# Kernel optimization log

Measured on AMD Instinct MI355X. Metric: run time of the kernel, lower is better.

## Reference

```python
import jax, jax.numpy as jnp
import numpy as np

B = 2048
IN_DIM = 98304
H1 = 256
H2 = 32


def setup_inputs() -> dict:
    key = jax.random.key(0)
    ks = jax.random.split(key, 7)
    # x emulates a sparse few-hot HalfKA feature vector: ~32 active features per row
    x = (jax.random.uniform(ks[0], (B, IN_DIM), dtype=jnp.float32) < (32.0 / IN_DIM)).astype(jnp.float32)
    s1 = 1.0 / np.sqrt(IN_DIM)
    s2 = 1.0 / np.sqrt(H1)
    s3 = 1.0 / np.sqrt(H2)
    return {
        "x": x,
        "W1": jax.random.normal(ks[1], (H1, IN_DIM), dtype=jnp.float32) * s1,
        "b1": jax.random.normal(ks[2], (H1,), dtype=jnp.float32) * s1,
        "W2": jax.random.normal(ks[3], (H2, H1), dtype=jnp.float32) * s2,
        "b2": jax.random.normal(ks[4], (H2,), dtype=jnp.float32) * s2,
        "Wout": jax.random.normal(ks[5], (1, H2), dtype=jnp.float32) * s3,
        "bout": jax.random.normal(ks[6], (1,), dtype=jnp.float32) * s3,
    }


def reference(x, W1, b1, W2, b2, Wout, bout):
    # fc1: [B, IN_DIM] @ [IN_DIM, H1] -> [B, H1]  (the sparse-accumulator hotspot)
    h1 = jax.nn.relu(jnp.dot(x, W1.T) + b1)
    h2 = jax.nn.relu(jnp.dot(h1, W2.T) + b2)
    out = jnp.dot(h2, Wout.T) + bout  # [B, 1]
    return out
```

## Files before the change

### kernel.cpp

```cpp
#include <hip/hip_runtime.h>

#define IN_DIM 98304
#define H1 256
#define H2 32
#define NZ_MAX 512
#define TS 64

typedef float f32x4 __attribute__((ext_vector_type(4)));
typedef unsigned short u16;
typedef u16 u16x4 __attribute__((ext_vector_type(4)));

__device__ __forceinline__ u16 f2bf(float f) {
    unsigned u = __builtin_bit_cast(unsigned, f);
    u = (u + 0x7FFFu + ((u >> 16) & 1u)) >> 16;
    return (u16)u;
}
__device__ __forceinline__ float bf2f(u16 h) {
    return __builtin_bit_cast(float, (unsigned)h << 16);
}

__global__ __launch_bounds__(256) void transpose_w1_bf16(const float* __restrict__ W1,
                                                         u16* __restrict__ W1T) {
    __shared__ float tile[TS][TS + 4];
    const int cb = blockIdx.x * TS;
    const int rb = blockIdx.y * TS;
    const int tx = threadIdx.x & 15;
    const int ty = threadIdx.x >> 4;

    #pragma unroll
    for (int rr = 0; rr < 4; ++rr) {
        const int r = rr * 16 + ty;
        f32x4 v = __builtin_nontemporal_load(reinterpret_cast<const f32x4*>(
            &W1[(size_t)(rb + r) * IN_DIM + cb + tx * 4]));
        tile[tx * 4 + 0][r] = v.x;
        tile[tx * 4 + 1][r] = v.y;
        tile[tx * 4 + 2][r] = v.z;
        tile[tx * 4 + 3][r] = v.w;
    }
    __syncthreads();
    #pragma unroll
    for (int cc = 0; cc < 4; ++cc) {
        const int c = cc * 16 + ty;
        u16x4 w;
        w.x = f2bf(tile[c][tx * 4 + 0]);
        w.y = f2bf(tile[c][tx * 4 + 1]);
        w.z = f2bf(tile[c][tx * 4 + 2]);
        w.w = f2bf(tile[c][tx * 4 + 3]);
        *reinterpret_cast<u16x4*>(&W1T[(size_t)(cb + c) * H1 + rb + tx * 4]) = w;
    }
}

template <bool USE_T>
__global__ __launch_bounds__(256) void nnue_fwd(
    const float* __restrict__ x,
    const float* __restrict__ W1,
    const u16*   __restrict__ W1T,
    const float* __restrict__ b1,
    const float* __restrict__ W2,
    const float* __restrict__ b2,
    const float* __restrict__ Wout,
    const float* __restrict__ bout,
    float* __restrict__ out)
{
    __shared__ int   s_idx[NZ_MAX];
    __shared__ float s_val[NZ_MAX];
    __shared__ float s_h1[H1];
    __shared__ float s_h2[H2];
    __shared__ int   s_cnt;

    const int tid = threadIdx.x;
    const int row = blockIdx.x;

    if (tid == 0) s_cnt = 0;
    __syncthreads();

    const f32x4* xr = reinterpret_cast<const f32x4*>(x + (size_t)row * IN_DIM);
    for (int o = 0; o < IN_DIM / (256 * 4 * 8); ++o) {
        f32x4 v[8];
        #pragma unroll
        for (int u = 0; u < 8; ++u)
            v[u] = __builtin_nontemporal_load(&xr[o * 2048 + u * 256 + tid]);
        #pragma unroll
        for (int u = 0; u < 8; ++u) {
            if (v[u].x != 0.f || v[u].y != 0.f || v[u].z != 0.f || v[u].w != 0.f) {
                const int col = (o * 2048 + u * 256 + tid) * 4;
                if (v[u].x != 0.f) { int p = atomicAdd(&s_cnt, 1); if (p < NZ_MAX) { s_idx[p] = col;     s_val[p] = v[u].x; } }
                if (v[u].y != 0.f) { int p = atomicAdd(&s_cnt, 1); if (p < NZ_MAX) { s_idx[p] = col + 1; s_val[p] = v[u].y; } }
                if (v[u].z != 0.f) { int p = atomicAdd(&s_cnt, 1); if (p < NZ_MAX) { s_idx[p] = col + 2; s_val[p] = v[u].z; } }
                if (v[u].w != 0.f) { int p = atomicAdd(&s_cnt, 1); if (p < NZ_MAX) { s_idx[p] = col + 3; s_val[p] = v[u].w; } }
            }
        }
    }
    __syncthreads();

    int cnt = s_cnt;
    if (cnt > NZ_MAX) cnt = NZ_MAX;
    const int cntp = (cnt + 3) & ~3;
    if (tid < cntp - cnt) { s_idx[cnt + tid] = 0; s_val[cnt + tid] = 0.f; }
    __syncthreads();

    {
        float acc = b1[tid];
        if (USE_T) {
            for (int k = 0; k < cntp; k += 4) {
                const int   i0 = s_idx[k + 0], i1 = s_idx[k + 1], i2 = s_idx[k + 2], i3 = s_idx[k + 3];
                const float c0 = s_val[k + 0], c1 = s_val[k + 1], c2 = s_val[k + 2], c3 = s_val[k + 3];
                const float a0 = bf2f(W1T[(size_t)i0 * H1 + tid]);
                const float a1 = bf2f(W1T[(size_t)i1 * H1 + tid]);
                const float a2 = bf2f(W1T[(size_t)i2 * H1 + tid]);
                const float a3 = bf2f(W1T[(size_t)i3 * H1 + tid]);
                acc += (c0 * a0 + c1 * a1) + (c2 * a2 + c3 * a3);
            }
        } else {
            const float* w1r = W1 + (size_t)tid * IN_DIM;
            for (int k = 0; k < cntp; k += 4) {
                const float a0 = s_val[k + 0] * w1r[s_idx[k + 0]];
                const float a1 = s_val[k + 1] * w1r[s_idx[k + 1]];
                const float a2 = s_val[k + 2] * w1r[s_idx[k + 2]];
                const float a3 = s_val[k + 3] * w1r[s_idx[k + 3]];
                acc += (a0 + a1) + (a2 + a3);
            }
        }
        s_h1[tid] = fmaxf(acc, 0.f);
    }
    __syncthreads();

    {
        const int j = tid >> 3;
        const int p = tid & 7;
        float part = 0.f;
        const float* w2r = W2 + j * H1 + p;
        #pragma unroll
        for (int k = 0; k < H1 / 8; ++k)
            part += w2r[8 * k] * s_h1[p + 8 * k];
        part += __shfl_xor(part, 1);
        part += __shfl_xor(part, 2);
        part += __shfl_xor(part, 4);
        if (p == 0) s_h2[j] = fmaxf(part + b2[j], 0.f);
    }
    __syncthreads();

    if (tid < 32) {
        float t = Wout[tid] * s_h2[tid];
        t += __shfl_xor(t, 1);
        t += __shfl_xor(t, 2);
        t += __shfl_xor(t, 4);
        t += __shfl_xor(t, 8);
        t += __shfl_xor(t, 16);
        if (tid == 0) out[row] = t + bout[0];
    }
}

extern "C" void kernel_launch(void* const* d_in, const int* in_sizes, int n_in,
                              void* d_out, int out_size, void* d_ws, size_t ws_size,
                              hipStream_t stream) {
    const float* x    = (const float*)d_in[0];
    const float* W1   = (const float*)d_in[1];
    const float* b1   = (const float*)d_in[2];
    const float* W2   = (const float*)d_in[3];
    const float* b2   = (const float*)d_in[4];
    const float* Wout = (const float*)d_in[5];
    const float* bout = (const float*)d_in[6];
    float* out = (float*)d_out;

    const int B = out_size;
    const size_t w1t_bytes = (size_t)IN_DIM * H1 * sizeof(u16);

    if (ws_size >= w1t_bytes) {
        u16* W1T = (u16*)d_ws;
        transpose_w1_bf16<<<dim3(IN_DIM / TS, H1 / TS), 256, 0, stream>>>(W1, W1T);
        nnue_fwd<true><<<B, 256, 0, stream>>>(x, W1, W1T, b1, W2, b2, Wout, bout, out);
    } else {
        nnue_fwd<false><<<B, 256, 0, stream>>>(x, W1, nullptr, b1, W2, b2, Wout, bout, out);
    }
}
```

Baseline: 170.2 us.

## Fuse W1 transpose and x scan into one cooperative kernel with grid sync

Adds a cooperative kernel with a grid of 1024 blocks. Each block transposes and converts six W1 tiles to bf16, then scans two x rows for nonzeros into shared memory, then waits at a grid-wide barrier before doing the sparse fc1 gather and the small MLP tail for its two rows. This overlaps the x scan with the W1 transpose and removes the second kernel launch. The cost is a grid sync, a 1024-block grid that must all be resident at once, and heavier shared memory per block; it falls back to the two-kernel path if the cooperative launch fails.

Result: slower. 465.6 us (+173.6%).

```diff
diff --git a/kernel.cpp b/kernel.cpp
--- a/kernel.cpp
+++ b/kernel.cpp
@@ -1,10 +1,14 @@
 #include <hip/hip_runtime.h>
+#include <hip/hip_cooperative_groups.h>
+
+namespace cg = cooperative_groups;
 
 #define IN_DIM 98304
 #define H1 256
 #define H2 32
 #define NZ_MAX 512
 #define TS 64
+#define COOP_GRID 1024
 
 typedef float f32x4 __attribute__((ext_vector_type(4)));
 typedef unsigned short u16;
@@ -17,6 +21,131 @@
 }
 __device__ __forceinline__ float bf2f(u16 h) {
     return __builtin_bit_cast(float, (unsigned)h << 16);
+}
+
+__global__ __launch_bounds__(256, 4) void nnue_coop(
+    const float* __restrict__ x, const float* __restrict__ W1,
+    u16* __restrict__ W1T, const float* __restrict__ b1,
+    const float* __restrict__ W2, const float* __restrict__ b2,
+    const float* __restrict__ Wout, const float* __restrict__ bout,
+    float* __restrict__ out)
+{
+    __shared__ __align__(16) float s_tile[TS][TS + 4];
+    __shared__ int   s_idx[2][NZ_MAX];
+    __shared__ float s_val[2][NZ_MAX];
+    __shared__ int   s_cnt[2];
+    __shared__ float s_h1[H1];
+    __shared__ float s_h2[H2];
+
+    const int tid = threadIdx.x;
+    const int b   = blockIdx.x;
+    const int tx  = tid & 15;
+    const int ty  = tid >> 4;
+
+    for (int i = 0; i < 6; ++i) {
+        const int t  = b * 6 + i;
+        const int cb = (t % (IN_DIM / TS)) * TS;
+        const int rb = (t / (IN_DIM / TS)) * TS;
+        __syncthreads();
+        #pragma unroll
+        for (int rr = 0; rr < 4; ++rr) {
+            const int r = rr * 16 + ty;
+            f32x4 v = __builtin_nontemporal_load(reinterpret_cast<const f32x4*>(
+                &W1[(size_t)(rb + r) * IN_DIM + cb + tx * 4]));
+            s_tile[tx * 4 + 0][r] = v.x;
+            s_tile[tx * 4 + 1][r] = v.y;
+            s_tile[tx * 4 + 2][r] = v.z;
+            s_tile[tx * 4 + 3][r] = v.w;
+        }
+        __syncthreads();
+        #pragma unroll
+        for (int cc = 0; cc < 4; ++cc) {
+            const int c = cc * 16 + ty;
+            u16x4 w;
+            w.x = f2bf(s_tile[c][tx * 4 + 0]);
+            w.y = f2bf(s_tile[c][tx * 4 + 1]);
+            w.z = f2bf(s_tile[c][tx * 4 + 2]);
+            w.w = f2bf(s_tile[c][tx * 4 + 3]);
+            *reinterpret_cast<u16x4*>(&W1T[(size_t)(cb + c) * H1 + rb + tx * 4]) = w;
+        }
+    }
+
+    if (tid == 0) { s_cnt[0] = 0; s_cnt[1] = 0; }
+    __syncthreads();
+    for (int r = 0; r < 2; ++r) {
+        const f32x4* xr = reinterpret_cast<const f32x4*>(x + (size_t)(b * 2 + r) * IN_DIM);
+        for (int o = 0; o < IN_DIM / (256 * 4 * 8); ++o) {
+            f32x4 v[8];
+            #pragma unroll
+            for (int u = 0; u < 8; ++u)
+                v[u] = __builtin_nontemporal_load(&xr[o * 2048 + u * 256 + tid]);
+            #pragma unroll
+            for (int u = 0; u < 8; ++u) {
+                if (v[u].x != 0.f || v[u].y != 0.f || v[u].z != 0.f || v[u].w != 0.f) {
+                    const int col = (o * 2048 + u * 256 + tid) * 4;
+                    if (v[u].x != 0.f) { int p = atomicAdd(&s_cnt[r], 1); if (p < NZ_MAX) { s_idx[r][p] = col;     s_val[r][p] = v[u].x; } }
+                    if (v[u].y != 0.f) { int p = atomicAdd(&s_cnt[r], 1); if (p < NZ_MAX) { s_idx[r][p] = col + 1; s_val[r][p] = v[u].y; } }
+                    if (v[u].z != 0.f) { int p = atomicAdd(&s_cnt[r], 1); if (p < NZ_MAX) { s_idx[r][p] = col + 2; s_val[r][p] = v[u].z; } }
+                    if (v[u].w != 0.f) { int p = atomicAdd(&s_cnt[r], 1); if (p < NZ_MAX) { s_idx[r][p] = col + 3; s_val[r][p] = v[u].w; } }
+                }
+            }
+        }
+    }
+    __syncthreads();
+    #pragma unroll
+    for (int r = 0; r < 2; ++r) {
+        int c = s_cnt[r]; if (c > NZ_MAX) c = NZ_MAX;
+        const int cp = (c + 3) & ~3;
+        if (tid < cp - c) { s_idx[r][c + tid] = 0; s_val[r][c + tid] = 0.f; }
+    }
+
+    __threadfence();
+    cg::this_grid().sync();
+
+    for (int r = 0; r < 2; ++r) {
+        const int row = b * 2 + r;
+        int cnt = s_cnt[r]; if (cnt > NZ_MAX) cnt = NZ_MAX;
+        const int cntp = (cnt + 3) & ~3;
+
+        float acc = b1[tid];
+        for (int k = 0; k < cntp; k += 4) {
+            const int   i0 = s_idx[r][k + 0], i1 = s_idx[r][k + 1], i2 = s_idx[r][k + 2], i3 = s_idx[r][k + 3];
+            const float c0 = s_val[r][k + 0], c1 = s_val[r][k + 1], c2 = s_val[r][k + 2], c3 = s_val[r][k + 3];
+            const float a0 = bf2f(W1T[(size_t)i0 * H1 + tid]);
+            const float a1 = bf2f(W1T[(size_t)i1 * H1 + tid]);
+            const float a2 = bf2f(W1T[(size_t)i2 * H1 + tid]);
+            const float a3 = bf2f(W1T[(size_t)i3 * H1 + tid]);
+            acc += (c0 * a0 + c1 * a1) + (c2 * a2 + c3 * a3);
+        }
+        s_h1[tid] = fmaxf(acc, 0.f);
+        __syncthreads();
+
+        {
+            const int j = tid >> 3;
+            const int p = tid & 7;
+            float part = 0.f;
+            const float* w2r = W2 + j * H1 + p;
+            #pragma unroll
+            for (int k = 0; k < H1 / 8; ++k)
+                part += w2r[8 * k] * s_h1[p + 8 * k];
+            part += __shfl_xor(part, 1);
+            part += __shfl_xor(part, 2);
+            part += __shfl_xor(part, 4);
+            if (p == 0) s_h2[j] = fmaxf(part + b2[j], 0.f);
+        }
+        __syncthreads();
+
+        if (tid < 32) {
+            float t = Wout[tid] * s_h2[tid];
+            t += __shfl_xor(t, 1);
+            t += __shfl_xor(t, 2);
+            t += __shfl_xor(t, 4);
+            t += __shfl_xor(t, 8);
+            t += __shfl_xor(t, 16);
+            if (tid == 0) out[row] = t + bout[0];
+        }
+        __syncthreads();
+    }
 }
 
 __global__ __launch_bounds__(256) void transpose_w1_bf16(const float* __restrict__ W1,
@@ -52,14 +181,10 @@
 
 template <bool USE_T>
 __global__ __launch_bounds__(256) void nnue_fwd(
-    const float* __restrict__ x,
-    const float* __restrict__ W1,
-    const u16*   __restrict__ W1T,
-    const float* __restrict__ b1,
-    const float* __restrict__ W2,
-    const float* __restrict__ b2,
-    const float* __restrict__ Wout,
-    const float* __restrict__ bout,
+    const float* __restrict__ x, const float* __restrict__ W1,
+    const u16* __restrict__ W1T, const float* __restrict__ b1,
+    const float* __restrict__ W2, const float* __restrict__ b2,
+    const float* __restrict__ Wout, const float* __restrict__ bout,
     float* __restrict__ out)
 {
     __shared__ int   s_idx[NZ_MAX];
@@ -168,8 +293,22 @@
 
     if (ws_size >= w1t_bytes) {
         u16* W1T = (u16*)d_ws;
-        transpose_w1_bf16<<<dim3(IN_DIM / TS, H1 / TS), 256, 0, stream>>>(W1, W1T);
-        nnue_fwd<true><<<B, 256, 0, stream>>>(x, W1, W1T, b1, W2, b2, Wout, bout, out);
+
+        bool coop_done = false;
+        if (B == COOP_GRID * 2) {
+            void* args[] = { (void*)&x, (void*)&W1, (void*)&W1T, (void*)&b1,
+                             (void*)&W2, (void*)&b2, (void*)&Wout, (void*)&bout,
+                             (void*)&out };
+            hipError_t e = hipLaunchCooperativeKernel(
+                reinterpret_cast<void*>(nnue_coop),
+                dim3(COOP_GRID), dim3(256), args, 0, stream);
+            if (e == hipSuccess) coop_done = true;
+            else (void)hipGetLastError();
+        }
+        if (!coop_done) {
+            transpose_w1_bf16<<<dim3(IN_DIM / TS, H1 / TS), 256, 0, stream>>>(W1, W1T);
+            nnue_fwd<true><<<B, 256, 0, stream>>>(x, W1, W1T, b1, W2, b2, Wout, bout, out);
+        }
     } else {
         nnue_fwd<false><<<B, 256, 0, stream>>>(x, W1, nullptr, b1, W2, b2, Wout, bout, out);
     }
```
